# Performance work log

Measured on AMD Instinct MI355X. Metric: run time of the kernel, lower is better.

Reference implementation:

```python
import jax, jax.numpy as jnp
import numpy as np

S = 32.0
M = 0.35
T = 0.2
EPS = 1e-12  # F.normalize default eps


def _l2_normalize(x, axis):
    n = jnp.sqrt(jnp.sum(x * x, axis=axis, keepdims=True))
    return x / jnp.maximum(n, EPS)


def setup_inputs() -> dict:
    key = jax.random.key(0)
    k1, k2, k3 = jax.random.split(key, 3)
    B, D, C = 512, 512, 100000
    return {
        "input": jax.random.normal(k1, (B, D), dtype=jnp.float32),
        "weight": jax.random.normal(k2, (C, D), dtype=jnp.float32),
        "label": jax.random.randint(k3, (B,), 0, C, dtype=jnp.int64),
    }


def reference(input, weight, label):
    B = input.shape[0]
    # normalized GEMM -> cosine similarities [B, C]
    cos_theta = _l2_normalize(input, 1) @ _l2_normalize(weight, 1).T
    cos_theta = jnp.clip(cos_theta, -1.0, 1.0)
    rows = jnp.arange(B)
    gt = cos_theta[rows, label][:, None]  # [B, 1]
    # MV-AM: boost hard (mis-classified-ish) logits: cos > gt - m
    hard = cos_theta > (gt - M)
    cos_theta = jnp.where(hard, (T + 1.0) * cos_theta + T, cos_theta)
    # easy_margin=False -> final_gt = gt - m; scatter into label column
    final_gt = gt - M
    cos_theta = cos_theta.at[rows, label].set(final_gt[:, 0])
    return cos_theta * S
```

## Files before the change

kernel.cpp:

```cpp
#include <hip/hip_runtime.h>
#include <hip/hip_bf16.h>


#define S_SCALE 32.0f
#define MARGIN  0.35f
#define T_BOOST 0.2f
#define EPSN    1e-12f

constexpr int Bn = 512;
constexpr int Dn = 512;
constexpr int Cn = 100000;
constexpr int BN = 64;

typedef __attribute__((ext_vector_type(8))) short bf16x8;
typedef __attribute__((ext_vector_type(4))) float f32x4;

static __device__ inline unsigned short f32_bf16(float f) {
    unsigned int u = __float_as_uint(f);
    u += 0x7FFFu + ((u >> 16) & 1u);
    return (unsigned short)(u >> 16);
}

__global__ __launch_bounds__(256) void prep_kernel(const float* __restrict__ in,
                                                   const float* __restrict__ w,
                                                   const int* __restrict__ label,
                                                   float* __restrict__ gt,
                                                   unsigned short* __restrict__ in_p) {
    int b = blockIdx.x, t = threadIdx.x;
    const float* irow = in + (size_t)b * Dn;
    int lab = label[b];
    const float* wrow = w + (size_t)lab * Dn;
    int c = 2 * t;
    float xa = irow[c], xb = irow[c + 1];
    float ya = wrow[c], yb = wrow[c + 1];
    float s_ii = xa*xa + xb*xb, s_ww = ya*ya + yb*yb, s_iw = xa*ya + xb*yb;
    #pragma unroll
    for (int off = 32; off; off >>= 1) {
        s_ii += __shfl_xor(s_ii, off);
        s_ww += __shfl_xor(s_ww, off);
        s_iw += __shfl_xor(s_iw, off);
    }
    __shared__ float r0[4], r1[4], r2[4], bc[1];
    int wid = t >> 6;
    if ((t & 63) == 0) { r0[wid] = s_ii; r1[wid] = s_ww; r2[wid] = s_iw; }
    __syncthreads();
    if (t == 0) {
        float a  = r0[0] + r0[1] + r0[2] + r0[3];
        float cc = r1[0] + r1[1] + r1[2] + r1[3];
        float d  = r2[0] + r2[1] + r2[2] + r2[3];
        float inv_i = 1.0f / fmaxf(sqrtf(a), EPSN);
        float g = d * inv_i / fmaxf(sqrtf(cc), EPSN);
        gt[b] = fminf(fmaxf(g, -1.0f), 1.0f);
        bc[0] = inv_i;
    }
    __syncthreads();
    float inv_i = bc[0];
    int g = b >> 4, l15 = b & 15;
    int s = t >> 4, lk = (t >> 2) & 3, j2 = (t & 3) * 4;
    int lane = lk * 16 + l15;
    unsigned int off = (unsigned)((g << 14) + (s << 10) + (lane << 4)) + j2;
    unsigned int h0 = f32_bf16(xa * inv_i), h1 = f32_bf16(xb * inv_i);
    *(unsigned int*)((char*)in_p + off) = h0 | (h1 << 16);
}

__global__ __launch_bounds__(512, 4) void gemm_kernel(const unsigned short* __restrict__ in_p,
                                                      const float* __restrict__ w,
                                                      const float* __restrict__ gt,
                                                      const int* __restrict__ label,
                                                      float* __restrict__ out) {
    __shared__ unsigned short Bs[BN * 512];
    char* bsb = (char*)Bs;
    int t = threadIdx.x, wid = t >> 6, lane = t & 63;
    int cbase = blockIdx.x * BN;

    {
        int rl = (wid << 3) | (lane >> 3);
        int rg = cbase + rl; if (rg >= Cn) rg = Cn - 1;
        const float* wr = w + (size_t)rg * Dn;
        int kc = lane & 7;
        float ssum = 0.f;
        #pragma unroll 4
        for (int q = 0; q < 16; ++q) {
            f32x4 v = *(const f32x4*)(wr + kc * 8 + (q >> 1) * 64 + (q & 1) * 4);
            ssum += v[0]*v[0] + v[1]*v[1] + v[2]*v[2] + v[3]*v[3];
        }
        ssum += __shfl_xor(ssum, 1); ssum += __shfl_xor(ssum, 2); ssum += __shfl_xor(ssum, 4);
        float invn = 1.0f / fmaxf(sqrtf(ssum), EPSN);
        #pragma unroll 2
        for (int i = 0; i < 8; ++i) {
            f32x4 v0 = *(const f32x4*)(wr + kc * 8 + i * 64);
            f32x4 v1 = *(const f32x4*)(wr + kc * 8 + i * 64 + 4);
            bf16x8 hv;
            #pragma unroll
            for (int j = 0; j < 4; ++j) {
                hv[j]     = (short)f32_bf16(v0[j] * invn);
                hv[4 + j] = (short)f32_bf16(v1[j] * invn);
            }
            unsigned int off = (unsigned)(((rl << 10) + (kc << 4) + (i << 7)) ^ ((rl & 7) << 4));
            *(bf16x8*)(bsb + off) = hv;
        }
    }
    __syncthreads();

    int l15 = lane & 15, lk = lane >> 4;
    const char* ap = (const char*)in_p + ((wid * 4) << 14) + (lane << 4);

    f32x4 acc[4][4];
    #pragma unroll
    for (int m = 0; m < 4; ++m)
        #pragma unroll
        for (int n = 0; n < 4; ++n) acc[m][n] = (f32x4){0.f, 0.f, 0.f, 0.f};

    bf16x8 a0[4], a1[4], bfrag[4];
    #pragma unroll
    for (int mf = 0; mf < 4; ++mf) a0[mf] = *(const bf16x8*)(ap + (mf << 14));

    for (int s2 = 0; s2 < 8; ++s2) {
        int se = s2 * 2, so = se + 1;
        #pragma unroll
        for (int mf = 0; mf < 4; ++mf)
            a1[mf] = *(const bf16x8*)(ap + (mf << 14) + (so << 10));
        #pragma unroll
        for (int nf = 0; nf < 4; ++nf) {
            int br = nf * 16 + l15;
            bfrag[nf] = *(const bf16x8*)(bsb + ((((br << 10) + (se << 6) + (lk << 4))) ^ ((br & 7) << 4)));
        }
        #pragma unroll
        for (int mf = 0; mf < 4; ++mf)
            #pragma unroll
            for (int nf = 0; nf < 4; ++nf)
                acc[mf][nf] = __builtin_amdgcn_mfma_f32_16x16x32_bf16(a0[mf], bfrag[nf], acc[mf][nf], 0, 0, 0);
        if (s2 < 7) {
            #pragma unroll
            for (int mf = 0; mf < 4; ++mf)
                a0[mf] = *(const bf16x8*)(ap + (mf << 14) + ((se + 2) << 10));
        }
        #pragma unroll
        for (int nf = 0; nf < 4; ++nf) {
            int br = nf * 16 + l15;
            bfrag[nf] = *(const bf16x8*)(bsb + ((((br << 10) + (so << 6) + (lk << 4))) ^ ((br & 7) << 4)));
        }
        #pragma unroll
        for (int mf = 0; mf < 4; ++mf)
            #pragma unroll
            for (int nf = 0; nf < 4; ++nf)
                acc[mf][nf] = __builtin_amdgcn_mfma_f32_16x16x32_bf16(a1[mf], bfrag[nf], acc[mf][nf], 0, 0, 0);
    }

    #pragma unroll
    for (int mf = 0; mf < 4; ++mf) {
        #pragma unroll
        for (int r = 0; r < 4; ++r) {
            int b_row = wid * 64 + mf * 16 + lk * 4 + r;
            float thr = gt[b_row] - MARGIN;
            int lab   = label[b_row];
            float gv  = thr * S_SCALE;
            size_t obase = (size_t)b_row * Cn;
            #pragma unroll
            for (int nf = 0; nf < 4; ++nf) {
                int c = cbase + nf * 16 + l15;
                if (c < Cn) {
                    float cosv = acc[mf][nf][r];
                    cosv = fminf(fmaxf(cosv, -1.0f), 1.0f);
                    float o = (cosv > thr) ? ((T_BOOST + 1.0f) * cosv + T_BOOST) : cosv;
                    o *= S_SCALE;
                    if (c == lab) o = gv;
                    __builtin_nontemporal_store(o, &out[obase + c]);
                }
            }
        }
    }
}

extern "C" void kernel_launch(void* const* d_in, const int* in_sizes, int n_in,
                              void* d_out, int out_size, void* d_ws, size_t ws_size,
                              hipStream_t stream) {
    const float* in  = (const float*)d_in[0];
    const float* w   = (const float*)d_in[1];
    const int* label = (const int*)d_in[2];
    float* out = (float*)d_out;

    char* ws = (char*)d_ws;
    float* gt            = (float*)ws;
    unsigned short* in_p = (unsigned short*)(ws + 4096);

    prep_kernel<<<dim3(Bn), dim3(256), 0, stream>>>(in, w, label, gt, in_p);
    gemm_kernel<<<dim3((Cn + BN - 1) / BN), dim3(512), 0, stream>>>(in_p, w, gt, label, out);
}
```

Measured before the change: 164.9 us.

## Single-pass weight load with deferred norm scaling and two-pass M tiling

The weight tile is now read from global memory once: the squared norm is accumulated while the raw values are converted to bf16 into LDS, and the inverse norm is applied to the accumulators in the epilogue. The GEMM is split into two passes over halves of the batch with a smaller 2x4 accumulator tile and a 5-deep rotating A-fragment prefetch. Output stores switch from nontemporal to plain stores. This removes a second global read of the weight rows and lowers register pressure, but the epilogue and output writes now run twice per block, and bf16 rounding of unnormalized weights may shift numerics slightly.

```diff
diff --git a/kernel.cpp b/kernel.cpp
--- a/kernel.cpp
+++ b/kernel.cpp
@@ -69,6 +69,7 @@
                                                       const int* __restrict__ label,
                                                       float* __restrict__ out) {
     __shared__ unsigned short Bs[BN * 512];
+    __shared__ float inv_s[BN];
     char* bsb = (char*)Bs;
     int t = threadIdx.x, wid = t >> 6, lane = t & 63;
     int cbase = blockIdx.x * BN;
@@ -79,93 +80,87 @@
         const float* wr = w + (size_t)rg * Dn;
         int kc = lane & 7;
         float ssum = 0.f;
-        #pragma unroll 4
-        for (int q = 0; q < 16; ++q) {
-            f32x4 v = *(const f32x4*)(wr + kc * 8 + (q >> 1) * 64 + (q & 1) * 4);
-            ssum += v[0]*v[0] + v[1]*v[1] + v[2]*v[2] + v[3]*v[3];
-        }
-        ssum += __shfl_xor(ssum, 1); ssum += __shfl_xor(ssum, 2); ssum += __shfl_xor(ssum, 4);
-        float invn = 1.0f / fmaxf(sqrtf(ssum), EPSN);
-        #pragma unroll 2
+        #pragma unroll
         for (int i = 0; i < 8; ++i) {
             f32x4 v0 = *(const f32x4*)(wr + kc * 8 + i * 64);
             f32x4 v1 = *(const f32x4*)(wr + kc * 8 + i * 64 + 4);
+            ssum += v0[0]*v0[0] + v0[1]*v0[1] + v0[2]*v0[2] + v0[3]*v0[3]
+                  + v1[0]*v1[0] + v1[1]*v1[1] + v1[2]*v1[2] + v1[3]*v1[3];
             bf16x8 hv;
             #pragma unroll
             for (int j = 0; j < 4; ++j) {
-                hv[j]     = (short)f32_bf16(v0[j] * invn);
-                hv[4 + j] = (short)f32_bf16(v1[j] * invn);
+                hv[j]     = (short)f32_bf16(v0[j]);
+                hv[4 + j] = (short)f32_bf16(v1[j]);
             }
             unsigned int off = (unsigned)(((rl << 10) + (kc << 4) + (i << 7)) ^ ((rl & 7) << 4));
             *(bf16x8*)(bsb + off) = hv;
         }
+        ssum += __shfl_xor(ssum, 1); ssum += __shfl_xor(ssum, 2); ssum += __shfl_xor(ssum, 4);
+        if (kc == 0) inv_s[rl] = 1.0f / fmaxf(sqrtf(ssum), EPSN);
     }
     __syncthreads();
 
     int l15 = lane & 15, lk = lane >> 4;
-    const char* ap = (const char*)in_p + ((wid * 4) << 14) + (lane << 4);
+    float invc[4];
+    #pragma unroll
+    for (int nf = 0; nf < 4; ++nf) invc[nf] = inv_s[nf * 16 + l15];
 
-    f32x4 acc[4][4];
-    #pragma unroll
-    for (int m = 0; m < 4; ++m)
+    for (int p = 0; p < 2; ++p) {
+        const char* ap = (const char*)in_p + ((size_t)((p * 16 + wid * 2) << 14)) + (lane << 4);
+
+        f32x4 acc[2][4];
         #pragma unroll
-        for (int n = 0; n < 4; ++n) acc[m][n] = (f32x4){0.f, 0.f, 0.f, 0.f};
+        for (int m = 0; m < 2; ++m)
+            #pragma unroll
+            for (int n = 0; n < 4; ++n) acc[m][n] = (f32x4){0.f, 0.f, 0.f, 0.f};
 
-    bf16x8 a0[4], a1[4], bfrag[4];
-    #pragma unroll
-    for (int mf = 0; mf < 4; ++mf) a0[mf] = *(const bf16x8*)(ap + (mf << 14));
+        bf16x8 ar[5][2];
+        #pragma unroll
+        for (int s = 0; s < 4; ++s)
+            #pragma unroll
+            for (int m = 0; m < 2; ++m)
+                ar[s][m] = *(const bf16x8*)(ap + (m << 14) + (s << 10));
 
-    for (int s2 = 0; s2 < 8; ++s2) {
-        int se = s2 * 2, so = se + 1;
         #pragma unroll
-        for (int mf = 0; mf < 4; ++mf)
-            a1[mf] = *(const bf16x8*)(ap + (mf << 14) + (so << 10));
-        #pragma unroll
-        for (int nf = 0; nf < 4; ++nf) {
-            int br = nf * 16 + l15;
-            bfrag[nf] = *(const bf16x8*)(bsb + ((((br << 10) + (se << 6) + (lk << 4))) ^ ((br & 7) << 4)));
-        }
-        #pragma unroll
-        for (int mf = 0; mf < 4; ++mf)
-            #pragma unroll
-            for (int nf = 0; nf < 4; ++nf)
-                acc[mf][nf] = __builtin_amdgcn_mfma_f32_16x16x32_bf16(a0[mf], bfrag[nf], acc[mf][nf], 0, 0, 0);
-        if (s2 < 7) {
-            #pragma unroll
-            for (int mf = 0; mf < 4; ++mf)
-                a0[mf] = *(const bf16x8*)(ap + (mf << 14) + ((se + 2) << 10));
-        }
-        #pragma unroll
-        for (int nf = 0; nf < 4; ++nf) {
-            int br = nf * 16 + l15;
-            bfrag[nf] = *(const bf16x8*)(bsb + ((((br << 10) + (so << 6) + (lk << 4))) ^ ((br & 7) << 4)));
-        }
-        #pragma unroll
-        for (int mf = 0; mf < 4; ++mf)
-            #pragma unroll
-            for (int nf = 0; nf < 4; ++nf)
-                acc[mf][nf] = __builtin_amdgcn_mfma_f32_16x16x32_bf16(a1[mf], bfrag[nf], acc[mf][nf], 0, 0, 0);
-    }
-
-    #pragma unroll
-    for (int mf = 0; mf < 4; ++mf) {
-        #pragma unroll
-        for (int r = 0; r < 4; ++r) {
-            int b_row = wid * 64 + mf * 16 + lk * 4 + r;
-            float thr = gt[b_row] - MARGIN;
-            int lab   = label[b_row];
-            float gv  = thr * S_SCALE;
-            size_t obase = (size_t)b_row * Cn;
+        for (int s = 0; s < 16; ++s) {
+            if (s + 4 < 16) {
+                #pragma unroll
+                for (int m = 0; m < 2; ++m)
+                    ar[(s + 4) % 5][m] = *(const bf16x8*)(ap + (m << 14) + ((s + 4) << 10));
+            }
+            bf16x8 bfrag[4];
             #pragma unroll
             for (int nf = 0; nf < 4; ++nf) {
-                int c = cbase + nf * 16 + l15;
-                if (c < Cn) {
-                    float cosv = acc[mf][nf][r];
-                    cosv = fminf(fmaxf(cosv, -1.0f), 1.0f);
-                    float o = (cosv > thr) ? ((T_BOOST + 1.0f) * cosv + T_BOOST) : cosv;
-                    o *= S_SCALE;
-                    if (c == lab) o = gv;
-                    __builtin_nontemporal_store(o, &out[obase + c]);
+                int br = nf * 16 + l15;
+                bfrag[nf] = *(const bf16x8*)(bsb + ((((br << 10) + (s << 6) + (lk << 4))) ^ ((br & 7) << 4)));
+            }
+            #pragma unroll
+            for (int m = 0; m < 2; ++m)
+                #pragma unroll
+                for (int nf = 0; nf < 4; ++nf)
+                    acc[m][nf] = __builtin_amdgcn_mfma_f32_16x16x32_bf16(ar[s % 5][m], bfrag[nf], acc[m][nf], 0, 0, 0);
+        }
+
+        #pragma unroll
+        for (int m = 0; m < 2; ++m) {
+            #pragma unroll
+            for (int r = 0; r < 4; ++r) {
+                int b_row = p * 256 + wid * 32 + m * 16 + lk * 4 + r;
+                float thr = gt[b_row] - MARGIN;
+                int lab   = label[b_row];
+                float gv  = thr * S_SCALE;
+                size_t obase = (size_t)b_row * Cn;
+                #pragma unroll
+                for (int nf = 0; nf < 4; ++nf) {
+                    int c = cbase + nf * 16 + l15;
+                    if (c < Cn) {
+                        float cosv = acc[m][nf][r] * invc[nf];
+                        cosv = fminf(fmaxf(cosv, -1.0f), 1.0f);
+                        float o = (cosv > thr) ? ((T_BOOST + 1.0f) * cosv + T_BOOST) : cosv;
+                        o *= S_SCALE;
+                        if (c == lab) o = gv;
+                        out[obase + c] = o;
+                    }
                 }
             }
         }
```

Result: slower. 476.8 us (+189.1%).
